# Optimization experiments

Measured on AMD Instinct MI355X. Metric: run time of the kernel, lower is better.

Reference implementation:

```python
import jax, jax.numpy as jnp
import numpy as np

R = 0.2          # stable-distribution hash bucket width
TABLE_SIZE = 2   # hash table size (buckets)
M = 5            # number of appended ALSH transform dims
EPS = 1e-12


def conv2d(x, W, b, pad):
    out = jax.lax.conv_general_dilated(
        x, W, window_strides=(1, 1), padding=[(pad, pad), (pad, pad)],
        dimension_numbers=('NCHW', 'OIHW', 'NCHW'))
    return out + b[None, :, None, None]


def maxpool2(x):
    return jax.lax.reduce_window(x, -jnp.inf, jax.lax.max,
                                 (1, 1, 2, 2), (1, 1, 2, 2), 'VALID')


def alsh_mask(x, W, a, c):
    """ALSH filter selection: hash P(kernels) and Q(query) with a stable
    distribution hash h(v)=floor((a.v+b)/r) mod table_size; active filters
    are those landing in the query's bucket. Returns [B, Cout] 0/1 mask.
    Multiplying conv output by this mask == gather active filters then
    zero_fill_missing back to full channel count."""
    Cout, Cin, kH, kW = W.shape
    Kf = W.reshape(Cout, -1)                       # [Cout, Cin*kH*kW]
    norms = jnp.linalg.norm(Kf, axis=1)
    Kn = Kf / (jnp.max(norms) + EPS)               # scale so all norms <= 1
    n = jnp.linalg.norm(Kn, axis=1, keepdims=True)
    # P transform: append norm^2, norm^4, ..., norm^(2^M)
    powers = jnp.concatenate([n ** (2 ** (i + 1)) for i in range(M)], axis=1)
    P = jnp.concatenate([Kn, powers], axis=1)      # [Cout, d+M]
    kh = jnp.mod(jnp.floor((P @ a + c[0]) / R), TABLE_SIZE)  # [Cout]
    # query vector: per-sample channel means broadcast over kernel support
    cm = x.mean(axis=(2, 3))                       # [B, Cin]
    q = jnp.repeat(cm, kH * kW, axis=1)            # [B, Cin*kH*kW] (cin,kh,kw order)
    qn = q / (jnp.linalg.norm(q, axis=1, keepdims=True) + EPS)
    # Q transform: append M halves
    Qv = jnp.concatenate([qn, jnp.full((q.shape[0], M), 0.5, q.dtype)], axis=1)
    qh = jnp.mod(jnp.floor((Qv @ a + c[0]) / R), TABLE_SIZE)  # [B]
    return (kh[None, :] == qh[:, None]).astype(x.dtype)       # [B, Cout]


def setup_inputs() -> dict:
    key = jax.random.key(0)
    ks = jax.random.split(key, 16)
    u = lambda k, s: jax.random.uniform(k, s, jnp.float32, 0.0, R)
    n = lambda k, s, sc=0.1: jax.random.normal(k, s, jnp.float32) * sc
    return {
        'x': jax.random.normal(ks[0], (4096, 3, 32, 32), jnp.float32),
        'W1': n(ks[1], (16, 3, 5, 5)), 'b1': n(ks[2], (16,)),
        'a1': jax.random.normal(ks[3], (80,), jnp.float32), 'c1': u(ks[4], (1,)),
        'W2': n(ks[5], (20, 16, 5, 5)), 'b2': n(ks[6], (20,)),
        'a2': jax.random.normal(ks[7], (405,), jnp.float32), 'c2': u(ks[8], (1,)),
        'W3': n(ks[9], (20, 20, 5, 5)), 'b3': n(ks[10], (20,)),
        'a3': jax.random.normal(ks[11], (505,), jnp.float32), 'c3': u(ks[12], (1,)),
        'Wo': n(ks[13], (10, 320)), 'bo': n(ks[14], (10,)),
    }


def reference(x, W1, b1, a1, c1, W2, b2, a2, c2, W3, b3, a3, c3, Wo, bo):
    m1 = alsh_mask(x, W1, a1, c1)
    h = jax.nn.relu(conv2d(x, W1, b1, 2)) * m1[:, :, None, None]
    h = maxpool2(h)                                # [B,16,16,16]
    m2 = alsh_mask(h, W2, a2, c2)
    h = jax.nn.relu(conv2d(h, W2, b2, 2)) * m2[:, :, None, None]
    h = maxpool2(h)                                # [B,20,8,8]
    m3 = alsh_mask(h, W3, a3, c3)
    h = jax.nn.relu(conv2d(h, W3, b3, 2)) * m3[:, :, None, None]
    # zero_fill_missing -> identity here: inactive channels already zero
    h = maxpool2(h)                                # [B,20,4,4]
    flat = h.reshape(h.shape[0], -1)               # [B,320]
    return flat @ Wo.T + bo
```

## Files before the change

kernel.cpp:

```cpp
#include <hip/hip_runtime.h>
#include <hip/hip_bf16.h>

#define EPSV 1e-12
#define RHASH 0.2

__device__ __forceinline__ int fmod2(double t) {
    return (int)(((long long)floor(t)) & 1LL);
}

__device__ void layer_setup(const float* W, const float* a, double cval,
                            int Co, int Ci, int* kh, double* asum, double* qc,
                            double* s_norm, float* Wbuf, float* abuf)
{
    const int t = threadIdx.x;
    const int D = Ci * 25;
    for (int i = t; i < Co * D; i += 256) Wbuf[i] = W[i];
    for (int i = t; i < D + 5; i += 256) abuf[i] = a[i];
    __syncthreads();
    if (t < Co) {
        double s = 0;
        for (int j = 0; j < D; ++j) { double w = (double)Wbuf[t * D + j]; s += w * w; }
        s_norm[t] = sqrt(s);
    }
    __syncthreads();
    if (t == 0) {
        double mx = 0;
        for (int i = 0; i < Co; ++i) mx = fmax(mx, s_norm[i]);
        s_norm[23] = 1.0 / (mx + EPSV);
    }
    __syncthreads();
    double scale = s_norm[23];
    if (t < Co) {
        double dp = 0;
        for (int j = 0; j < D; ++j) dp += (double)Wbuf[t * D + j] * (double)abuf[j];
        dp *= scale;
        double n = s_norm[t] * scale;
        double p = n * n;
        for (int m = 0; m < 5; ++m) { dp += p * (double)abuf[D + m]; p *= p; }
        kh[t] = fmod2((dp + cval) / RHASH);
    }
    if (t >= 64 && t < 64 + Ci) {
        int c = t - 64;
        double s = 0;
        for (int j = 0; j < 25; ++j) s += (double)abuf[c * 25 + j];
        asum[c] = s;
    }
    if (t == 128) {
        double s = 0;
        for (int m = 0; m < 5; ++m) s += (double)abuf[D + m];
        *qc = 0.5 * s + cval;
    }
    __syncthreads();
}

__global__ __launch_bounds__(256) void setup_kernel(
    const float* W1, const float* a1, const float* c1,
    const float* W2, const float* a2, const float* c2,
    const float* W3, const float* a3, const float* c3,
    double* dmeta, int* imeta)
{
    __shared__ float Wbuf[10000];
    __shared__ float abuf[512];
    __shared__ double s_norm[24];
    layer_setup(W1, a1, (double)c1[0], 16, 3,  imeta + 0,  dmeta + 0,  dmeta + 39, s_norm, Wbuf, abuf);
    layer_setup(W2, a2, (double)c2[0], 20, 16, imeta + 16, dmeta + 3,  dmeta + 40, s_norm, Wbuf, abuf);
    layer_setup(W3, a3, (double)c3[0], 20, 20, imeta + 36, dmeta + 19, dmeta + 41, s_norm, Wbuf, abuf);
}

__global__ __launch_bounds__(256) void pack_kernel(const float* W1, const float* W2, const float* W3,
                                                   float* Wp1, float* Wp2, float* Wp3)
{
    int i = blockIdx.x * 256 + threadIdx.x;
    if (i < 1200) {
        int co = i & 15, r = i >> 4;
        int kx = r % 5, r2 = r / 5, ky = r2 % 5, ci = r2 / 5;
        Wp1[i] = W1[co * 75 + ci * 25 + ky * 5 + kx];
    } else if (i < 1200 + 8960) {
        int k = i - 1200;
        int j = k % 28, r = k / 28;
        int cog = r % 4, r2 = r / 4, ky = r2 % 5, ci = r2 / 5;
        Wp2[k] = (j < 25) ? W2[(cog * 5 + j / 5) * 400 + ci * 25 + ky * 5 + (j % 5)] : 0.f;
    } else if (i < 1200 + 8960 + 11200) {
        int k = i - 10160;
        int j = k % 28, r = k / 28;
        int cog = r % 4, r2 = r / 4, ky = r2 % 5, ci = r2 / 5;
        Wp3[k] = (j < 25) ? W3[(cog * 5 + j / 5) * 500 + ci * 25 + ky * 5 + (j % 5)] : 0.f;
    }
}

__global__ __launch_bounds__(256) void hq1_kernel(const float* __restrict__ x,
    const double* __restrict__ dmeta, int* __restrict__ qh1, int B)
{
    int b = blockIdx.x * 4 + (threadIdx.x >> 6);
    int ln = threadIdx.x & 63;
    if (b >= B) return;
    const float4* xb = (const float4*)(x + (size_t)b * 3072);
    double dp = 0, nn = 0;
    for (int c = 0; c < 3; ++c) {
        double s = 0;
        #pragma unroll
        for (int j = 0; j < 4; ++j) {
            float4 v = xb[c * 256 + ln + 64 * j];
            s += (double)v.x + (double)v.y + (double)v.z + (double)v.w;
        }
        #pragma unroll
        for (int off = 32; off; off >>= 1) s += __shfl_xor(s, off);
        double cm = s * (1.0 / 1024.0);
        dp += cm * dmeta[c]; nn += cm * cm;
    }
    int qh = fmod2((dp / (5.0 * sqrt(nn) + EPSV) + dmeta[39]) / RHASH);
    if (ln == 0) qh1[b] = qh;
}

__global__ __launch_bounds__(256) void hq2_kernel(const float* __restrict__ h1,
    const double* __restrict__ dmeta, int* __restrict__ qh2, int B)
{
    int b = blockIdx.x * 4 + (threadIdx.x >> 6);
    int ln = threadIdx.x & 63;
    if (b >= B) return;
    const float4* hb = (const float4*)(h1 + (size_t)b * 4096);
    double dp = 0, nn = 0;
    for (int c = 0; c < 16; ++c) {
        float4 v = hb[c * 64 + ln];
        double s = (double)v.x + (double)v.y + (double)v.z + (double)v.w;
        #pragma unroll
        for (int off = 32; off; off >>= 1) s += __shfl_xor(s, off);
        double cm = s * (1.0 / 256.0);
        dp += cm * dmeta[3 + c]; nn += cm * cm;
    }
    int qh = fmod2((dp / (5.0 * sqrt(nn) + EPSV) + dmeta[40]) / RHASH);
    if (ln == 0) qh2[b] = qh;
}

__global__ __launch_bounds__(256) void hq3_kernel(const float* __restrict__ h2,
    const double* __restrict__ dmeta, int* __restrict__ qh3, int B)
{
    int b = blockIdx.x * 4 + (threadIdx.x >> 6);
    int ln = threadIdx.x & 63;
    if (b >= B) return;
    const float4* hb = (const float4*)(h2 + (size_t)b * 1280);
    int g = ln >> 4;
    double dp = 0, nn = 0;
    #pragma unroll
    for (int j = 0; j < 5; ++j) {
        float4 v = hb[ln + 64 * j];
        double s = (double)v.x + (double)v.y + (double)v.z + (double)v.w;
        #pragma unroll
        for (int off = 1; off < 16; off <<= 1) s += __shfl_xor(s, off);
        int c = g + 4 * j;
        double cm = s * (1.0 / 64.0);
        dp += cm * dmeta[19 + c]; nn += cm * cm;
    }
    dp += __shfl_xor(dp, 16); dp += __shfl_xor(dp, 32);
    nn += __shfl_xor(nn, 16); nn += __shfl_xor(nn, 32);
    int qh = fmod2((dp / (5.0 * sqrt(nn) + EPSV) + dmeta[41]) / RHASH);
    if (ln == 0) qh3[b] = qh;
}

__global__ __launch_bounds__(256) void conv1_kernel(
    const float* __restrict__ x, const float* __restrict__ Wp1,
    const float* __restrict__ b1, const int* __restrict__ kh1,
    const int* __restrict__ qh1, float* __restrict__ h1)
{
    __shared__ float xs[3][36][36];
    __shared__ float Ws[1200];

    const int b = blockIdx.x, t = threadIdx.x;

    for (int i = t; i < 3 * 36 * 36; i += 256) (&xs[0][0][0])[i] = 0.f;
    for (int i = t; i < 600; i += 256) ((float2*)Ws)[i] = ((const float2*)Wp1)[i];
    __syncthreads();
    const float2* xb2 = (const float2*)(x + (size_t)b * 3072);
    for (int i = t; i < 1536; i += 256) {
        int idx = i * 2, c = idx >> 10, rem = idx & 1023;
        *(float2*)&xs[c][(rem >> 5) + 2][(rem & 31) + 2] = xb2[i];
    }
    __syncthreads();

    const int qh = qh1[b];
    const int py = t >> 4, px = t & 15;
    const int y0 = 2 * py, x0 = 2 * px;

    float acc[16][4];
    #pragma unroll
    for (int c = 0; c < 16; ++c) {
        float bb = b1[c];
        acc[c][0] = bb; acc[c][1] = bb; acc[c][2] = bb; acc[c][3] = bb;
    }
    #pragma unroll
    for (int ci = 0; ci < 3; ++ci) {
        #pragma unroll
        for (int ky = 0; ky < 5; ++ky) {
            float xr0[6], xr1[6];
            {
                float2 a0 = *(const float2*)&xs[ci][y0 + ky][x0];
                float2 a1 = *(const float2*)&xs[ci][y0 + ky][x0 + 2];
                float2 a2 = *(const float2*)&xs[ci][y0 + ky][x0 + 4];
                float2 c0 = *(const float2*)&xs[ci][y0 + ky + 1][x0];
                float2 c1 = *(const float2*)&xs[ci][y0 + ky + 1][x0 + 2];
                float2 c2 = *(const float2*)&xs[ci][y0 + ky + 1][x0 + 4];
                xr0[0]=a0.x; xr0[1]=a0.y; xr0[2]=a1.x; xr0[3]=a1.y; xr0[4]=a2.x; xr0[5]=a2.y;
                xr1[0]=c0.x; xr1[1]=c0.y; xr1[2]=c1.x; xr1[3]=c1.y; xr1[4]=c2.x; xr1[5]=c2.y;
            }
            const float* wbase = Ws + ((ci * 5 + ky) * 5) * 16;
            #pragma unroll
            for (int kx = 0; kx < 5; ++kx) {
                float wc[16];
                const float4* wp = (const float4*)(wbase + kx * 16);
                *(float4*)&wc[0]  = wp[0];
                *(float4*)&wc[4]  = wp[1];
                *(float4*)&wc[8]  = wp[2];
                *(float4*)&wc[12] = wp[3];
                #pragma unroll
                for (int c = 0; c < 16; ++c) {
                    acc[c][0] = fmaf(wc[c], xr0[kx],     acc[c][0]);
                    acc[c][1] = fmaf(wc[c], xr0[kx + 1], acc[c][1]);
                    acc[c][2] = fmaf(wc[c], xr1[kx],     acc[c][2]);
                    acc[c][3] = fmaf(wc[c], xr1[kx + 1], acc[c][3]);
                }
            }
        }
    }
    float* hb = h1 + (size_t)b * 4096 + t;
    #pragma unroll
    for (int c = 0; c < 16; ++c) {
        float m = fmaxf(fmaxf(acc[c][0], acc[c][1]), fmaxf(acc[c][2], acc[c][3]));
        hb[c * 256] = fmaxf(m, 0.f) * ((kh1[c] == qh) ? 1.f : 0.f);
    }
}

__global__ __launch_bounds__(256) void conv2_kernel(
    const float* __restrict__ h1, const float* __restrict__ Wp2,
    const float* __restrict__ b2, const int* __restrict__ kh2,
    const int* __restrict__ qh2, float* __restrict__ h2)
{
    __shared__ float xs[8][20][20];
    __shared__ float Ws[4480];

    const int b = blockIdx.x, t = threadIdx.x;
    const int cog = t >> 6, pos = t & 63;
    const int py = pos >> 3, px = pos & 7;
    const int y0 = 2 * py, x0 = 2 * px;

    for (int i = t; i < 8 * 20 * 20; i += 256) (&xs[0][0][0])[i] = 0.f;

    const int qh = qh2[b];
    float acc[5][4];
    #pragma unroll
    for (int c = 0; c < 5; ++c) {
        float bb = b2[cog * 5 + c];
        acc[c][0] = bb; acc[c][1] = bb; acc[c][2] = bb; acc[c][3] = bb;
    }
    __syncthreads();

    for (int ch = 0; ch < 2; ++ch) {
        for (int i = t; i < 2240; i += 256)
            ((float2*)Ws)[i] = ((const float2*)(Wp2 + ch * 4480))[i];
        const float2* src = (const float2*)(h1 + (size_t)b * 4096 + ch * 2048);
        for (int i = t; i < 1024; i += 256) {
            int ci = i >> 7, r = i & 127, p2 = r * 2;
            *(float2*)&xs[ci][(p2 >> 4) + 2][(p2 & 15) + 2] = src[i];
        }
        __syncthreads();

        for (int ci = 0; ci < 8; ++ci) {
            #pragma unroll
            for (int ky = 0; ky < 5; ++ky) {
                float xr0[6], xr1[6];
                {
                    float2 a0 = *(const float2*)&xs[ci][y0 + ky][x0];
                    float2 a1 = *(const float2*)&xs[ci][y0 + ky][x0 + 2];
                    float2 a2 = *(const float2*)&xs[ci][y0 + ky][x0 + 4];
                    float2 c0 = *(const float2*)&xs[ci][y0 + ky + 1][x0];
                    float2 c1 = *(const float2*)&xs[ci][y0 + ky + 1][x0 + 2];
                    float2 c2 = *(const float2*)&xs[ci][y0 + ky + 1][x0 + 4];
                    xr0[0]=a0.x; xr0[1]=a0.y; xr0[2]=a1.x; xr0[3]=a1.y; xr0[4]=a2.x; xr0[5]=a2.y;
                    xr1[0]=c0.x; xr1[1]=c0.y; xr1[2]=c1.x; xr1[3]=c1.y; xr1[4]=c2.x; xr1[5]=c2.y;
                }
                float wv[28];
                const float4* wp = (const float4*)&Ws[((ci * 5 + ky) * 4 + cog) * 28];
                *(float4*)&wv[0]  = wp[0];
                *(float4*)&wv[4]  = wp[1];
                *(float4*)&wv[8]  = wp[2];
                *(float4*)&wv[12] = wp[3];
                *(float4*)&wv[16] = wp[4];
                *(float4*)&wv[20] = wp[5];
                *(float4*)&wv[24] = wp[6];
                #pragma unroll
                for (int c = 0; c < 5; ++c) {
                    #pragma unroll
                    for (int kx = 0; kx < 5; ++kx) {
                        float w = wv[c * 5 + kx];
                        acc[c][0] = fmaf(w, xr0[kx],     acc[c][0]);
                        acc[c][1] = fmaf(w, xr0[kx + 1], acc[c][1]);
                        acc[c][2] = fmaf(w, xr1[kx],     acc[c][2]);
                        acc[c][3] = fmaf(w, xr1[kx + 1], acc[c][3]);
                    }
                }
            }
        }
        __syncthreads();
    }

    float* ob = h2 + (size_t)b * 1280 + pos;
    #pragma unroll
    for (int c = 0; c < 5; ++c) {
        int co = cog * 5 + c;
        float m = fmaxf(fmaxf(acc[c][0], acc[c][1]), fmaxf(acc[c][2], acc[c][3]));
        ob[co * 64] = fmaxf(m, 0.f) * ((kh2[co] == qh) ? 1.f : 0.f);
    }
}

__global__ __launch_bounds__(256) void conv3_kernel(
    const float* __restrict__ h2, const float* __restrict__ Wp3,
    const float* __restrict__ b3, const int* __restrict__ kh3,
    const int* __restrict__ qh3,
    const float* __restrict__ Wo, const float* __restrict__ bo,
    float* __restrict__ out, int B)
{
    __shared__ float xs[4][5][12][12];
    __shared__ float Ws[2800];
    __shared__ float flat[4][320];

    const int b0 = blockIdx.x * 4, t = threadIdx.x;
    const int s = t >> 6, q = t & 63, cog = q >> 4, pos = q & 15;
    const int py = pos >> 2, px = pos & 3;
    const int y0 = 2 * py, x0 = 2 * px;
    const int b = b0 + s;

    for (int i = t; i < 4 * 5 * 144; i += 256) (&xs[0][0][0][0])[i] = 0.f;

    const int qh = (b < B) ? qh3[b] : 0;
    float acc[5][4];
    #pragma unroll
    for (int c = 0; c < 5; ++c) {
        float bb = b3[cog * 5 + c];
        acc[c][0] = bb; acc[c][1] = bb; acc[c][2] = bb; acc[c][3] = bb;
    }
    __syncthreads();

    for (int ch = 0; ch < 4; ++ch) {
        for (int i = t; i < 1400; i += 256)
            ((float2*)Ws)[i] = ((const float2*)(Wp3 + ch * 2800))[i];
        for (int i = t; i < 640; i += 256) {
            int ss = i / 160, r = i - ss * 160, ci = r >> 5, rr = r & 31, p2 = rr * 2;
            if (b0 + ss < B)
                *(float2*)&xs[ss][ci][(p2 >> 3) + 2][(p2 & 7) + 2] =
                    ((const float2*)(h2 + (size_t)(b0 + ss) * 1280 + (ch * 5 + ci) * 64))[rr];
        }
        __syncthreads();

        #pragma unroll
        for (int ci = 0; ci < 5; ++ci) {
            #pragma unroll
            for (int ky = 0; ky < 5; ++ky) {
                float xr0[6], xr1[6];
                {
                    float2 a0 = *(const float2*)&xs[s][ci][y0 + ky][x0];
                    float2 a1 = *(const float2*)&xs[s][ci][y0 + ky][x0 + 2];
                    float2 a2 = *(const float2*)&xs[s][ci][y0 + ky][x0 + 4];
                    float2 c0 = *(const float2*)&xs[s][ci][y0 + ky + 1][x0];
                    float2 c1 = *(const float2*)&xs[s][ci][y0 + ky + 1][x0 + 2];
                    float2 c2 = *(const float2*)&xs[s][ci][y0 + ky + 1][x0 + 4];
                    xr0[0]=a0.x; xr0[1]=a0.y; xr0[2]=a1.x; xr0[3]=a1.y; xr0[4]=a2.x; xr0[5]=a2.y;
                    xr1[0]=c0.x; xr1[1]=c0.y; xr1[2]=c1.x; xr1[3]=c1.y; xr1[4]=c2.x; xr1[5]=c2.y;
                }
                float wv[28];
                const float4* wp = (const float4*)&Ws[((ci * 5 + ky) * 4 + cog) * 28];
                *(float4*)&wv[0]  = wp[0];
                *(float4*)&wv[4]  = wp[1];
                *(float4*)&wv[8]  = wp[2];
                *(float4*)&wv[12] = wp[3];
                *(float4*)&wv[16] = wp[4];
                *(float4*)&wv[20] = wp[5];
                *(float4*)&wv[24] = wp[6];
                #pragma unroll
                for (int c = 0; c < 5; ++c) {
                    #pragma unroll
                    for (int kx = 0; kx < 5; ++kx) {
                        float w = wv[c * 5 + kx];
                        acc[c][0] = fmaf(w, xr0[kx],     acc[c][0]);
                        acc[c][1] = fmaf(w, xr0[kx + 1], acc[c][1]);
                        acc[c][2] = fmaf(w, xr1[kx],     acc[c][2]);
                        acc[c][3] = fmaf(w, xr1[kx + 1], acc[c][3]);
                    }
                }
            }
        }
        __syncthreads();
    }

    #pragma unroll
    for (int c = 0; c < 5; ++c) {
        int co = cog * 5 + c;
        float m = fmaxf(fmaxf(acc[c][0], acc[c][1]), fmaxf(acc[c][2], acc[c][3]));
        flat[s][co * 16 + pos] = fmaxf(m, 0.f) * ((kh3[co] == qh) ? 1.f : 0.f);
    }
    __syncthreads();

    if (t < 160) {
        const int g = t >> 2, qq = t & 3;
        const int ss = g / 10, o = g - ss * 10;
        float a = 0.f;
        const float* wr = Wo + o * 320;
        for (int k = qq; k < 320; k += 4) a = fmaf(flat[ss][k], wr[k], a);
        a += __shfl_xor(a, 1);
        a += __shfl_xor(a, 2);
        if (qq == 0 && b0 + ss < B) out[(size_t)(b0 + ss) * 10 + o] = a + bo[o];
    }
}

extern "C" void kernel_launch(void* const* d_in, const int* in_sizes, int n_in,
                              void* d_out, int out_size, void* d_ws, size_t ws_size,
                              hipStream_t stream)
{
    const float* x  = (const float*)d_in[0];
    const float* W1 = (const float*)d_in[1];
    const float* b1 = (const float*)d_in[2];
    const float* a1 = (const float*)d_in[3];
    const float* c1 = (const float*)d_in[4];
    const float* W2 = (const float*)d_in[5];
    const float* b2 = (const float*)d_in[6];
    const float* a2 = (const float*)d_in[7];
    const float* c2 = (const float*)d_in[8];
    const float* W3 = (const float*)d_in[9];
    const float* b3 = (const float*)d_in[10];
    const float* a3 = (const float*)d_in[11];
    const float* c3 = (const float*)d_in[12];
    const float* Wo = (const float*)d_in[13];
    const float* bo = (const float*)d_in[14];
    float* out = (float*)d_out;

    const int B = in_sizes[0] / 3072;

    float* h1  = (float*)d_ws;
    float* h2  = h1 + (size_t)B * 4096;
    float* Wp1 = h2 + (size_t)B * 1280;
    float* Wp2 = Wp1 + 1200;
    float* Wp3 = Wp2 + 8960;
    double* dmeta = (double*)(Wp3 + 11200);
    int* imeta = (int*)(dmeta + 42);
    int* qh1 = imeta + 56;
    int* qh2 = qh1 + B;
    int* qh3 = qh2 + B;

    setup_kernel<<<1, 256, 0, stream>>>(W1, a1, c1, W2, a2, c2, W3, a3, c3, dmeta, imeta);
    pack_kernel<<<84, 256, 0, stream>>>(W1, W2, W3, Wp1, Wp2, Wp3);
    hq1_kernel<<<(B + 3) / 4, 256, 0, stream>>>(x, dmeta, qh1, B);
    conv1_kernel<<<B, 256, 0, stream>>>(x, Wp1, b1, imeta, qh1, h1);
    hq2_kernel<<<(B + 3) / 4, 256, 0, stream>>>(h1, dmeta, qh2, B);
    conv2_kernel<<<B, 256, 0, stream>>>(h1, Wp2, b2, imeta + 16, qh2, h2);
    hq3_kernel<<<(B + 3) / 4, 256, 0, stream>>>(h2, dmeta, qh3, B);
    conv3_kernel<<<(B + 3) / 4, 256, 0, stream>>>(h2, Wp3, b3, imeta + 36, qh3, Wo, bo, out, B);
}
```

Baseline: 558.3 us.

## Fuse query-hash reductions into conv epilogues and slide input rows in registers

Removes the three separate hash-query kernels. Layer-1 channel means are computed from the shared-memory input tile inside conv1, and the next layer's query hash is computed from each conv's pooled output in its epilogue using wave shuffles plus a block reduction. The conv inner loops now keep a sliding pair of 6-float rows in registers, so each row is read from LDS once rather than twice, and the shared tiles get padded row strides. This saves three kernel launches and the re-reads of h1 and h2 from global memory, at the cost of extra syncs and shuffle work in each conv block.

```diff
diff --git a/kernel.cpp b/kernel.cpp
--- a/kernel.cpp
+++ b/kernel.cpp
@@ -6,6 +6,13 @@
 
 __device__ __forceinline__ int fmod2(double t) {
     return (int)(((long long)floor(t)) & 1LL);
+}
+
+__device__ __forceinline__ void load_row6(const float* base, float* r) {
+    float2 a0 = *(const float2*)(base);
+    float2 a1 = *(const float2*)(base + 2);
+    float2 a2 = *(const float2*)(base + 4);
+    r[0] = a0.x; r[1] = a0.y; r[2] = a1.x; r[3] = a1.y; r[4] = a2.x; r[5] = a2.y;
 }
 
 __device__ void layer_setup(const float* W, const float* a, double cval,
@@ -88,86 +95,21 @@
     }
 }
 
-__global__ __launch_bounds__(256) void hq1_kernel(const float* __restrict__ x,
-    const double* __restrict__ dmeta, int* __restrict__ qh1, int B)
-{
-    int b = blockIdx.x * 4 + (threadIdx.x >> 6);
-    int ln = threadIdx.x & 63;
-    if (b >= B) return;
-    const float4* xb = (const float4*)(x + (size_t)b * 3072);
-    double dp = 0, nn = 0;
-    for (int c = 0; c < 3; ++c) {
-        double s = 0;
-        #pragma unroll
-        for (int j = 0; j < 4; ++j) {
-            float4 v = xb[c * 256 + ln + 64 * j];
-            s += (double)v.x + (double)v.y + (double)v.z + (double)v.w;
-        }
-        #pragma unroll
-        for (int off = 32; off; off >>= 1) s += __shfl_xor(s, off);
-        double cm = s * (1.0 / 1024.0);
-        dp += cm * dmeta[c]; nn += cm * cm;
-    }
-    int qh = fmod2((dp / (5.0 * sqrt(nn) + EPSV) + dmeta[39]) / RHASH);
-    if (ln == 0) qh1[b] = qh;
-}
-
-__global__ __launch_bounds__(256) void hq2_kernel(const float* __restrict__ h1,
-    const double* __restrict__ dmeta, int* __restrict__ qh2, int B)
-{
-    int b = blockIdx.x * 4 + (threadIdx.x >> 6);
-    int ln = threadIdx.x & 63;
-    if (b >= B) return;
-    const float4* hb = (const float4*)(h1 + (size_t)b * 4096);
-    double dp = 0, nn = 0;
-    for (int c = 0; c < 16; ++c) {
-        float4 v = hb[c * 64 + ln];
-        double s = (double)v.x + (double)v.y + (double)v.z + (double)v.w;
-        #pragma unroll
-        for (int off = 32; off; off >>= 1) s += __shfl_xor(s, off);
-        double cm = s * (1.0 / 256.0);
-        dp += cm * dmeta[3 + c]; nn += cm * cm;
-    }
-    int qh = fmod2((dp / (5.0 * sqrt(nn) + EPSV) + dmeta[40]) / RHASH);
-    if (ln == 0) qh2[b] = qh;
-}
-
-__global__ __launch_bounds__(256) void hq3_kernel(const float* __restrict__ h2,
-    const double* __restrict__ dmeta, int* __restrict__ qh3, int B)
-{
-    int b = blockIdx.x * 4 + (threadIdx.x >> 6);
-    int ln = threadIdx.x & 63;
-    if (b >= B) return;
-    const float4* hb = (const float4*)(h2 + (size_t)b * 1280);
-    int g = ln >> 4;
-    double dp = 0, nn = 0;
-    #pragma unroll
-    for (int j = 0; j < 5; ++j) {
-        float4 v = hb[ln + 64 * j];
-        double s = (double)v.x + (double)v.y + (double)v.z + (double)v.w;
-        #pragma unroll
-        for (int off = 1; off < 16; off <<= 1) s += __shfl_xor(s, off);
-        int c = g + 4 * j;
-        double cm = s * (1.0 / 64.0);
-        dp += cm * dmeta[19 + c]; nn += cm * cm;
-    }
-    dp += __shfl_xor(dp, 16); dp += __shfl_xor(dp, 32);
-    nn += __shfl_xor(nn, 16); nn += __shfl_xor(nn, 32);
-    int qh = fmod2((dp / (5.0 * sqrt(nn) + EPSV) + dmeta[41]) / RHASH);
-    if (ln == 0) qh3[b] = qh;
-}
-
 __global__ __launch_bounds__(256) void conv1_kernel(
     const float* __restrict__ x, const float* __restrict__ Wp1,
     const float* __restrict__ b1, const int* __restrict__ kh1,
-    const int* __restrict__ qh1, float* __restrict__ h1)
-{
-    __shared__ float xs[3][36][36];
+    const double* __restrict__ dmeta, float* __restrict__ h1,
+    int* __restrict__ qh2)
+{
+    __shared__ float xs[3][36][38];
     __shared__ float Ws[1200];
+    __shared__ double s_red[3];
+    __shared__ double s_ch[16][4];
 
     const int b = blockIdx.x, t = threadIdx.x;
-
-    for (int i = t; i < 3 * 36 * 36; i += 256) (&xs[0][0][0])[i] = 0.f;
+    const int w = t >> 6, ln = t & 63;
+
+    for (int i = t; i < 3 * 36 * 38; i += 256) (&xs[0][0][0])[i] = 0.f;
     for (int i = t; i < 600; i += 256) ((float2*)Ws)[i] = ((const float2*)Wp1)[i];
     __syncthreads();
     const float2* xb2 = (const float2*)(x + (size_t)b * 3072);
@@ -177,7 +119,25 @@
     }
     __syncthreads();
 
-    const int qh = qh1[b];
+    if (w < 3) {
+        double s = 0;
+        for (int j = 0; j < 16; ++j) {
+            int i = ln + 64 * j;
+            s += (double)xs[w][(i >> 5) + 2][(i & 31) + 2];
+        }
+        #pragma unroll
+        for (int off = 32; off; off >>= 1) s += __shfl_xor(s, off);
+        if (ln == 0) s_red[w] = s;
+    }
+    __syncthreads();
+    double dp = 0, nn = 0;
+    #pragma unroll
+    for (int c = 0; c < 3; ++c) {
+        double cm = s_red[c] * (1.0 / 1024.0);
+        dp += cm * dmeta[c]; nn += cm * cm;
+    }
+    const int qh = fmod2((dp / (5.0 * sqrt(nn) + EPSV) + dmeta[39]) / RHASH);
+
     const int py = t >> 4, px = t & 15;
     const int y0 = 2 * py, x0 = 2 * px;
 
@@ -189,19 +149,11 @@
     }
     #pragma unroll
     for (int ci = 0; ci < 3; ++ci) {
+        float cur[6], nxt[6];
+        load_row6(&xs[ci][y0][x0], cur);
+        load_row6(&xs[ci][y0 + 1][x0], nxt);
         #pragma unroll
         for (int ky = 0; ky < 5; ++ky) {
-            float xr0[6], xr1[6];
-            {
-                float2 a0 = *(const float2*)&xs[ci][y0 + ky][x0];
-                float2 a1 = *(const float2*)&xs[ci][y0 + ky][x0 + 2];
-                float2 a2 = *(const float2*)&xs[ci][y0 + ky][x0 + 4];
-                float2 c0 = *(const float2*)&xs[ci][y0 + ky + 1][x0];
-                float2 c1 = *(const float2*)&xs[ci][y0 + ky + 1][x0 + 2];
-                float2 c2 = *(const float2*)&xs[ci][y0 + ky + 1][x0 + 4];
-                xr0[0]=a0.x; xr0[1]=a0.y; xr0[2]=a1.x; xr0[3]=a1.y; xr0[4]=a2.x; xr0[5]=a2.y;
-                xr1[0]=c0.x; xr1[1]=c0.y; xr1[2]=c1.x; xr1[3]=c1.y; xr1[4]=c2.x; xr1[5]=c2.y;
-            }
             const float* wbase = Ws + ((ci * 5 + ky) * 5) * 16;
             #pragma unroll
             for (int kx = 0; kx < 5; ++kx) {
@@ -213,36 +165,63 @@
                 *(float4*)&wc[12] = wp[3];
                 #pragma unroll
                 for (int c = 0; c < 16; ++c) {
-                    acc[c][0] = fmaf(wc[c], xr0[kx],     acc[c][0]);
-                    acc[c][1] = fmaf(wc[c], xr0[kx + 1], acc[c][1]);
-                    acc[c][2] = fmaf(wc[c], xr1[kx],     acc[c][2]);
-                    acc[c][3] = fmaf(wc[c], xr1[kx + 1], acc[c][3]);
+                    acc[c][0] = fmaf(wc[c], cur[kx],     acc[c][0]);
+                    acc[c][1] = fmaf(wc[c], cur[kx + 1], acc[c][1]);
+                    acc[c][2] = fmaf(wc[c], nxt[kx],     acc[c][2]);
+                    acc[c][3] = fmaf(wc[c], nxt[kx + 1], acc[c][3]);
                 }
             }
-        }
-    }
+            if (ky < 4) {
+                #pragma unroll
+                for (int j = 0; j < 6; ++j) cur[j] = nxt[j];
+                load_row6(&xs[ci][y0 + ky + 2][x0], nxt);
+            }
+        }
+    }
+
+    float mv[16];
     float* hb = h1 + (size_t)b * 4096 + t;
     #pragma unroll
     for (int c = 0; c < 16; ++c) {
         float m = fmaxf(fmaxf(acc[c][0], acc[c][1]), fmaxf(acc[c][2], acc[c][3]));
-        hb[c * 256] = fmaxf(m, 0.f) * ((kh1[c] == qh) ? 1.f : 0.f);
+        mv[c] = fmaxf(m, 0.f) * ((kh1[c] == qh) ? 1.f : 0.f);
+        hb[c * 256] = mv[c];
+    }
+    #pragma unroll
+    for (int c = 0; c < 16; ++c) {
+        double s = (double)mv[c];
+        #pragma unroll
+        for (int off = 32; off; off >>= 1) s += __shfl_xor(s, off);
+        if (ln == 0) s_ch[c][w] = s;
+    }
+    __syncthreads();
+    if (t == 0) {
+        double dp2 = 0, nn2 = 0;
+        #pragma unroll
+        for (int c = 0; c < 16; ++c) {
+            double cm = (s_ch[c][0] + s_ch[c][1] + s_ch[c][2] + s_ch[c][3]) * (1.0 / 256.0);
+            dp2 += cm * dmeta[3 + c]; nn2 += cm * cm;
+        }
+        qh2[b] = fmod2((dp2 / (5.0 * sqrt(nn2) + EPSV) + dmeta[40]) / RHASH);
     }
 }
 
 __global__ __launch_bounds__(256) void conv2_kernel(
     const float* __restrict__ h1, const float* __restrict__ Wp2,
     const float* __restrict__ b2, const int* __restrict__ kh2,
-    const int* __restrict__ qh2, float* __restrict__ h2)
-{
-    __shared__ float xs[8][20][20];
+    const int* __restrict__ qh2, const double* __restrict__ dmeta,
+    float* __restrict__ h2, int* __restrict__ qh3)
+{
+    __shared__ float xs[8][20][22];
     __shared__ float Ws[4480];
+    __shared__ double s_ch[20];
 
     const int b = blockIdx.x, t = threadIdx.x;
     const int cog = t >> 6, pos = t & 63;
     const int py = pos >> 3, px = pos & 7;
     const int y0 = 2 * py, x0 = 2 * px;
 
-    for (int i = t; i < 8 * 20 * 20; i += 256) (&xs[0][0][0])[i] = 0.f;
+    for (int i = t; i < 8 * 20 * 22; i += 256) (&xs[0][0][0])[i] = 0.f;
 
     const int qh = qh2[b];
     float acc[5][4];
@@ -264,19 +243,11 @@
         __syncthreads();
 
         for (int ci = 0; ci < 8; ++ci) {
+            float cur[6], nxt[6];
+            load_row6(&xs[ci][y0][x0], cur);
+            load_row6(&xs[ci][y0 + 1][x0], nxt);
             #pragma unroll
             for (int ky = 0; ky < 5; ++ky) {
-                float xr0[6], xr1[6];
-                {
-                    float2 a0 = *(const float2*)&xs[ci][y0 + ky][x0];
-                    float2 a1 = *(const float2*)&xs[ci][y0 + ky][x0 + 2];
-                    float2 a2 = *(const float2*)&xs[ci][y0 + ky][x0 + 4];
-                    float2 c0 = *(const float2*)&xs[ci][y0 + ky + 1][x0];
-                    float2 c1 = *(const float2*)&xs[ci][y0 + ky + 1][x0 + 2];
-                    float2 c2 = *(const float2*)&xs[ci][y0 + ky + 1][x0 + 4];
-                    xr0[0]=a0.x; xr0[1]=a0.y; xr0[2]=a1.x; xr0[3]=a1.y; xr0[4]=a2.x; xr0[5]=a2.y;
-                    xr1[0]=c0.x; xr1[1]=c0.y; xr1[2]=c1.x; xr1[3]=c1.y; xr1[4]=c2.x; xr1[5]=c2.y;
-                }
                 float wv[28];
                 const float4* wp = (const float4*)&Ws[((ci * 5 + ky) * 4 + cog) * 28];
                 *(float4*)&wv[0]  = wp[0];
@@ -290,24 +261,48 @@
                 for (int c = 0; c < 5; ++c) {
                     #pragma unroll
                     for (int kx = 0; kx < 5; ++kx) {
-                        float w = wv[c * 5 + kx];
-                        acc[c][0] = fmaf(w, xr0[kx],     acc[c][0]);
-                        acc[c][1] = fmaf(w, xr0[kx + 1], acc[c][1]);
-                        acc[c][2] = fmaf(w, xr1[kx],     acc[c][2]);
-                        acc[c][3] = fmaf(w, xr1[kx + 1], acc[c][3]);
+                        float wgt = wv[c * 5 + kx];
+                        acc[c][0] = fmaf(wgt, cur[kx],     acc[c][0]);
+                        acc[c][1] = fmaf(wgt, cur[kx + 1], acc[c][1]);
+                        acc[c][2] = fmaf(wgt, nxt[kx],     acc[c][2]);
+                        acc[c][3] = fmaf(wgt, nxt[kx + 1], acc[c][3]);
                     }
                 }
+                if (ky < 4) {
+                    #pragma unroll
+                    for (int j = 0; j < 6; ++j) cur[j] = nxt[j];
+                    load_row6(&xs[ci][y0 + ky + 2][x0], nxt);
+                }
             }
         }
         __syncthreads();
     }
 
+    float mv[5];
     float* ob = h2 + (size_t)b * 1280 + pos;
     #pragma unroll
     for (int c = 0; c < 5; ++c) {
         int co = cog * 5 + c;
         float m = fmaxf(fmaxf(acc[c][0], acc[c][1]), fmaxf(acc[c][2], acc[c][3]));
-        ob[co * 64] = fmaxf(m, 0.f) * ((kh2[co] == qh) ? 1.f : 0.f);
+        mv[c] = fmaxf(m, 0.f) * ((kh2[co] == qh) ? 1.f : 0.f);
+        ob[co * 64] = mv[c];
+    }
+    #pragma unroll
+    for (int c = 0; c < 5; ++c) {
+        double s = (double)mv[c];
+        #pragma unroll
+        for (int off = 32; off; off >>= 1) s += __shfl_xor(s, off);
+        if (pos == 0) s_ch[cog * 5 + c] = s;
+    }
+    __syncthreads();
+    if (t == 0) {
+        double dp = 0, nn = 0;
+        #pragma unroll
+        for (int c = 0; c < 20; ++c) {
+            double cm = s_ch[c] * (1.0 / 64.0);
+            dp += cm * dmeta[19 + c]; nn += cm * cm;
+        }
+        qh3[b] = fmod2((dp / (5.0 * sqrt(nn) + EPSV) + dmeta[41]) / RHASH);
     }
 }
 
@@ -318,7 +313,7 @@
     const float* __restrict__ Wo, const float* __restrict__ bo,
     float* __restrict__ out, int B)
 {
-    __shared__ float xs[4][5][12][12];
+    __shared__ float xs[4][5][12][14];
     __shared__ float Ws[2800];
     __shared__ float flat[4][320];
 
@@ -328,7 +323,7 @@
     const int y0 = 2 * py, x0 = 2 * px;
     const int b = b0 + s;
 
-    for (int i = t; i < 4 * 5 * 144; i += 256) (&xs[0][0][0][0])[i] = 0.f;
+    for (int i = t; i < 4 * 5 * 12 * 14; i += 256) (&xs[0][0][0][0])[i] = 0.f;
 
     const int qh = (b < B) ? qh3[b] : 0;
     float acc[5][4];
@@ -352,19 +347,11 @@
 
         #pragma unroll
         for (int ci = 0; ci < 5; ++ci) {
+            float cur[6], nxt[6];
+            load_row6(&xs[s][ci][y0][x0], cur);
+            load_row6(&xs[s][ci][y0 + 1][x0], nxt);
             #pragma unroll
             for (int ky = 0; ky < 5; ++ky) {
-                float xr0[6], xr1[6];
-                {
-                    float2 a0 = *(const float2*)&xs[s][ci][y0 + ky][x0];
-                    float2 a1 = *(const float2*)&xs[s][ci][y0 + ky][x0 + 2];
-                    float2 a2 = *(const float2*)&xs[s][ci][y0 + ky][x0 + 4];
-                    float2 c0 = *(const float2*)&xs[s][ci][y0 + ky + 1][x0];
-                    float2 c1 = *(const float2*)&xs[s][ci][y0 + ky + 1][x0 + 2];
-                    float2 c2 = *(const float2*)&xs[s][ci][y0 + ky + 1][x0 + 4];
-                    xr0[0]=a0.x; xr0[1]=a0.y; xr0[2]=a1.x; xr0[3]=a1.y; xr0[4]=a2.x; xr0[5]=a2.y;
-                    xr1[0]=c0.x; xr1[1]=c0.y; xr1[2]=c1.x; xr1[3]=c1.y; xr1[4]=c2.x; xr1[5]=c2.y;
-                }
                 float wv[28];
                 const float4* wp = (const float4*)&Ws[((ci * 5 + ky) * 4 + cog) * 28];
                 *(float4*)&wv[0]  = wp[0];
@@ -378,12 +365,17 @@
                 for (int c = 0; c < 5; ++c) {
                     #pragma unroll
                     for (int kx = 0; kx < 5; ++kx) {
-                        float w = wv[c * 5 + kx];
-                        acc[c][0] = fmaf(w, xr0[kx],     acc[c][0]);
-                        acc[c][1] = fmaf(w, xr0[kx + 1], acc[c][1]);
-                        acc[c][2] = fmaf(w, xr1[kx],     acc[c][2]);
-                        acc[c][3] = fmaf(w, xr1[kx + 1], acc[c][3]);
+                        float wgt = wv[c * 5 + kx];
+                        acc[c][0] = fmaf(wgt, cur[kx],     acc[c][0]);
+                        acc[c][1] = fmaf(wgt, cur[kx + 1], acc[c][1]);
+                        acc[c][2] = fmaf(wgt, nxt[kx],     acc[c][2]);
+                        acc[c][3] = fmaf(wgt, nxt[kx + 1], acc[c][3]);
                     }
+                }
+                if (ky < 4) {
+                    #pragma unroll
+                    for (int j = 0; j < 6; ++j) cur[j] = nxt[j];
+                    load_row6(&xs[s][ci][y0 + ky + 2][x0], nxt);
                 }
             }
         }
@@ -440,16 +432,12 @@
     float* Wp3 = Wp2 + 8960;
     double* dmeta = (double*)(Wp3 + 11200);
     int* imeta = (int*)(dmeta + 42);
-    int* qh1 = imeta + 56;
-    int* qh2 = qh1 + B;
+    int* qh2 = imeta + 56;
     int* qh3 = qh2 + B;
 
     setup_kernel<<<1, 256, 0, stream>>>(W1, a1, c1, W2, a2, c2, W3, a3, c3, dmeta, imeta);
     pack_kernel<<<84, 256, 0, stream>>>(W1, W2, W3, Wp1, Wp2, Wp3);
-    hq1_kernel<<<(B + 3) / 4, 256, 0, stream>>>(x, dmeta, qh1, B);
-    conv1_kernel<<<B, 256, 0, stream>>>(x, Wp1, b1, imeta, qh1, h1);
-    hq2_kernel<<<(B + 3) / 4, 256, 0, stream>>>(h1, dmeta, qh2, B);
-    conv2_kernel<<<B, 256, 0, stream>>>(h1, Wp2, b2, imeta + 16, qh2, h2);
-    hq3_kernel<<<(B + 3) / 4, 256, 0, stream>>>(h2, dmeta, qh3, B);
+    conv1_kernel<<<B, 256, 0, stream>>>(x, Wp1, b1, imeta, dmeta, h1, qh2);
+    conv2_kernel<<<B, 256, 0, stream>>>(h1, Wp2, b2, imeta + 16, qh2, dmeta, h2, qh3);
     conv3_kernel<<<(B + 3) / 4, 256, 0, stream>>>(h2, Wp3, b3, imeta + 36, qh3, Wo, bo, out, B);
 }
```

Measured after the change: 567.3 us. No clear change (+1.6%).
